# Kernel tuning notes

Hardware: AMD Instinct MI355X
Metric: run time of the kernel (lower is better)

Reference implementation:

```python
import jax, jax.numpy as jnp
import numpy as np

H, KVH, HD = 32, 8, 128          # query heads, kv heads, head_dim
HIDDEN = H * HD                   # 4096
TOTAL_KV = 3072                   # sum of (start_pos + seqlen) over the batch (static)
ROPE_THETA = 10000.0


def setup_inputs() -> dict:
    key = jax.random.key(0)
    ks = jax.random.split(key, 4)
    x = jax.random.normal(ks[0], (1024, HIDDEN), jnp.float32)
    wqkv = jax.random.normal(ks[1], (HIDDEN, HIDDEN + 2 * KVH * HD), jnp.float32) * 0.02
    wo = jax.random.normal(ks[2], (HIDDEN, HIDDEN), jnp.float32) * 0.02
    # paged cache: [num_layers=1, 2(k/v), cache_slots, kv_heads, head_dim], holds post-RoPE prefixes
    kv_cache = jax.random.normal(ks[3], (1, 2, 8192, KVH, HD), jnp.float32) * 0.02
    # 4 ragged requests: seqlens [512,256,128,128], cached prefixes [0,512,1024,512]
    seqstarts = jnp.array([0, 512, 768, 896, 1024], jnp.int32)
    start_pos = jnp.array([0, 512, 1024, 512], jnp.int32)
    kvstarts = jnp.array([0, 512, 1280, 2432, 3072], jnp.int32)  # cumsum of start_pos+seqlen
    cachestarts = jnp.array([0, 1024, 2560, 4096], jnp.int32)    # page base per request
    return dict(x=x, wqkv=wqkv, wo=wo, kv_cache=kv_cache, seqstarts=seqstarts,
                kvstarts=kvstarts, cachestarts=cachestarts, start_pos=start_pos)


def _rope(t, pos):
    # interleaved (GPT-J style) rotary over full head_dim; t: [T, nheads, HD], pos: [T]
    d2 = HD // 2
    inv_freq = 1.0 / (ROPE_THETA ** (jnp.arange(d2, dtype=jnp.float32) / d2))
    ang = pos.astype(jnp.float32)[:, None] * inv_freq      # [T, d2]
    cos = jnp.cos(ang)[:, None, :]
    sin = jnp.sin(ang)[:, None, :]
    x1, x2 = t[..., 0::2], t[..., 1::2]
    r1 = x1 * cos - x2 * sin
    r2 = x1 * sin + x2 * cos
    return jnp.stack([r1, r2], axis=-1).reshape(t.shape)


def _forward(x, wqkv, wo, kv_cache, seqstarts, kvstarts, cachestarts, start_pos):
    T = x.shape[0]
    # fused QKV projection
    xqkv = (x @ wqkv).reshape(T, H + 2 * KVH, HD)
    xq, xk, xv = jnp.split(xqkv, [H, H + KVH], axis=1)   # [T,32,HD],[T,8,HD],[T,8,HD]

    # per-token batch id and absolute position (ragged via seqstarts)
    tok = jnp.arange(T)
    bq = jnp.searchsorted(seqstarts, tok, side='right') - 1
    pos_q = tok - seqstarts[bq] + start_pos[bq]
    xq = _rope(xq, pos_q)
    xk = _rope(xk, pos_q)

    # assemble ragged KV stream: cached prefix (paged cache) + freshly projected tokens
    kvtok = jnp.arange(TOTAL_KV)
    bkv = jnp.searchsorted(kvstarts, kvtok, side='right') - 1
    pkv = kvtok - kvstarts[bkv]                              # absolute kv position
    is_new = pkv >= start_pos[bkv]
    new_idx = jnp.clip(seqstarts[bkv] + pkv - start_pos[bkv], 0, T - 1)
    cache_idx = cachestarts[bkv] + pkv                       # paged slot for prefix
    keys = jnp.where(is_new[:, None, None], xk[new_idx], kv_cache[0, 0][cache_idx])
    vals = jnp.where(is_new[:, None, None], xv[new_idx], kv_cache[0, 1][cache_idx])

    # GQA: repeat kv heads to match query heads
    rep = H // KVH
    keys = jnp.repeat(keys, rep, axis=1)                     # [TOTAL_KV, 32, HD]
    vals = jnp.repeat(vals, rep, axis=1)

    scale = 1.0 / jnp.sqrt(jnp.float32(HD))
    scores = jnp.einsum('qhd,khd->hqk', xq, keys) * scale    # [32, T, TOTAL_KV]
    # ragged causal mask: same request and kv position <= query position
    mask = (bq[:, None] == bkv[None, :]) & (pkv[None, :] <= pos_q[:, None])
    scores = jnp.where(mask[None], scores, jnp.float32(-1e30))
    probs = jax.nn.softmax(scores, axis=-1)
    attn = jnp.einsum('hqk,khd->qhd', probs, vals)           # [T, 32, HD]
    return attn.reshape(T, HIDDEN) @ wo


def reference(x, wqkv, wo, kv_cache, seqstarts, kvstarts, cachestarts, start_pos):
    return _forward(x, wqkv, wo, kv_cache, seqstarts, kvstarts, cachestarts, start_pos)
```

## Files before the change

kernel.cpp:

```cpp
#include <hip/hip_runtime.h>
#include <hip/hip_bf16.h>
#include <math.h>
#include <stdint.h>

typedef __bf16 bf16;
typedef __attribute__((ext_vector_type(4))) float floatx4;
typedef __attribute__((ext_vector_type(8))) bf16 bf16x8;
typedef __attribute__((ext_vector_type(4))) bf16 bf16x4;

#define LDS_ASYNC16(gptr, lptr)                                                \
  __builtin_amdgcn_global_load_lds(                                            \
      (const __attribute__((address_space(1))) void*)(gptr),                   \
      (__attribute__((address_space(3))) void*)(lptr), 16, 0, 0)

__global__ __launch_bounds__(256) void k_cvt(const float* __restrict__ in,
                                             bf16* __restrict__ out) {
  int i = (blockIdx.x * 256 + threadIdx.x) * 4;
  float4 v = *(const float4*)(in + i);
  bf16x4 o;
  o[0] = (bf16)v.x; o[1] = (bf16)v.y; o[2] = (bf16)v.z; o[3] = (bf16)v.w;
  *(bf16x4*)(out + i) = o;
}

__global__ __launch_bounds__(256) void k_merge(const float* __restrict__ a,
                                               const float* __restrict__ b,
                                               float* __restrict__ out) {
  int i = (blockIdx.x * 256 + threadIdx.x) * 4;
  float4 va = *(const float4*)(a + i);
  float4 vb = *(const float4*)(b + i);
  float4 o;
  o.x = va.x + vb.x; o.y = va.y + vb.y; o.z = va.z + vb.z; o.w = va.w + vb.w;
  *(float4*)(out + i) = o;
}

__global__ __launch_bounds__(256) void k_transpose_cvt(const float* __restrict__ in,
                                                       bf16* __restrict__ out,
                                                       int K, int N) {
  __shared__ float tile[64][65];
  int k0 = blockIdx.y * 64, n0 = blockIdx.x * 64;
  int tid = threadIdx.x;
  int cg = tid & 15, rr = tid >> 4;
#pragma unroll
  for (int p = 0; p < 4; ++p) {
    int r = rr + p * 16;
    float4 v = *(const float4*)(in + (size_t)(k0 + r) * N + n0 + cg * 4);
    tile[r][cg * 4 + 0] = v.x; tile[r][cg * 4 + 1] = v.y;
    tile[r][cg * 4 + 2] = v.z; tile[r][cg * 4 + 3] = v.w;
  }
  __syncthreads();
#pragma unroll
  for (int p = 0; p < 4; ++p) {
    int n = rr + p * 16;
    bf16x4 o;
    o[0] = (bf16)tile[cg * 4 + 0][n];
    o[1] = (bf16)tile[cg * 4 + 1][n];
    o[2] = (bf16)tile[cg * 4 + 2][n];
    o[3] = (bf16)tile[cg * 4 + 3][n];
    *(bf16x4*)(out + (size_t)(n0 + n) * K + k0 + cg * 4) = o;
  }
}

__global__ __launch_bounds__(256) void k_gemm_bt(const bf16* __restrict__ A,
                                                 const bf16* __restrict__ B,
                                                 float* __restrict__ C,
                                                 int M, int N, int K, int ksplit) {
  __shared__ bf16 As[128 * 32];
  __shared__ bf16 Bs[128 * 32];
  int tid = threadIdx.x;
  int w = tid >> 6, lane = tid & 63;
  int lq = lane >> 4, l16 = lane & 15;
  int bm = blockIdx.y * 128, bn = blockIdx.x * 128;
  int wm = (w >> 1) * 64, wn = (w & 1) * 64;
  int kc = K / ksplit;
  int koff = blockIdx.z * kc;
  C += (size_t)blockIdx.z * M * N;
  floatx4 acc[4][4] = {};
  const bf16* Ab = A + (size_t)bm * K;
  const bf16* Bb = B + (size_t)bn * K;
  int srow = (lane >> 2);
  int scol = (lane & 3) * 8;

  for (int k0 = koff; k0 < koff + kc; k0 += 32) {
#pragma unroll
    for (int c = 0; c < 2; ++c) {
      int r = w * 32 + c * 16 + srow;
      LDS_ASYNC16(Ab + (size_t)r * K + k0 + scol, &As[(w * 32 + c * 16) * 32]);
      LDS_ASYNC16(Bb + (size_t)r * K + k0 + scol, &Bs[(w * 32 + c * 16) * 32]);
    }
    __syncthreads();
    bf16x8 af[4], bfr[4];
#pragma unroll
    for (int i = 0; i < 4; ++i)
      af[i] = *(const bf16x8*)&As[(wm + i * 16 + l16) * 32 + lq * 8];
#pragma unroll
    for (int j = 0; j < 4; ++j)
      bfr[j] = *(const bf16x8*)&Bs[(wn + j * 16 + l16) * 32 + lq * 8];
#pragma unroll
    for (int i = 0; i < 4; ++i)
#pragma unroll
      for (int j = 0; j < 4; ++j)
        acc[i][j] = __builtin_amdgcn_mfma_f32_16x16x32_bf16(af[i], bfr[j],
                                                            acc[i][j], 0, 0, 0);
    __syncthreads();
  }
#pragma unroll
  for (int i = 0; i < 4; ++i)
#pragma unroll
    for (int j = 0; j < 4; ++j) {
      int m = bm + wm + i * 16 + lq * 4;
      int n = bn + wn + j * 16 + l16;
      float* cp = C + (size_t)m * N + n;
#pragma unroll
      for (int r = 0; r < 4; ++r) cp[(size_t)r * N] = acc[i][j][r];
    }
}

__global__ __launch_bounds__(256) void k_rope(const float* __restrict__ xp0,
                                              const float* __restrict__ xp1,
                                              bf16* __restrict__ qb,
                                              bf16* __restrict__ kb,
                                              const int* __restrict__ seqstarts,
                                              const int* __restrict__ start_pos) {
  int t = blockIdx.x;
  int s = 0;
  for (int i = 1; i < 4; ++i) if (seqstarts[i] <= t) s = i;
  float pos = (float)(t - seqstarts[s] + start_pos[s]);
  for (int wk = threadIdx.x; wk < 40 * 64; wk += 256) {
    int hh = wk >> 6, j = wk & 63;
    size_t idx = ((size_t)t * 48 + hh) * 128 + 2 * j;
    float x1 = xp0[idx] + xp1[idx];
    float x2 = xp0[idx + 1] + xp1[idx + 1];
    float invf = exp2f(-(float)j * 0.20762050593045935f);
    float ang = pos * invf;
    float sv, cv;
    sincosf(ang, &sv, &cv);
    float r1 = x1 * cv - x2 * sv;
    float r2 = x1 * sv + x2 * cv;
    unsigned int u1 = (unsigned int)__builtin_bit_cast(unsigned short, (bf16)r1);
    unsigned int u2 = (unsigned int)__builtin_bit_cast(unsigned short, (bf16)r2);
    unsigned int pk = u1 | (u2 << 16);
    unsigned int* dst = (hh < 32)
        ? (unsigned int*)(qb + ((size_t)t * 32 + hh) * 128)
        : (unsigned int*)(kb + ((size_t)t * 8 + (hh - 32)) * 128);
    dst[j] = pk;
  }
}

__global__ __launch_bounds__(256) void k_assemble_k(
    const bf16* __restrict__ xk, const float* __restrict__ ck,
    bf16* __restrict__ kall,
    const int* __restrict__ seqstarts, const int* __restrict__ kvstarts,
    const int* __restrict__ cachestarts, const int* __restrict__ start_pos) {
  int p = blockIdx.x;
  int b = 0;
  for (int i = 1; i < 4; ++i) if (kvstarts[i] <= p) b = i;
  int pkv = p - kvstarts[b];
  int tid = threadIdx.x;
  int hk = tid >> 5, d4 = (tid & 31) * 4;
  bf16* dst = kall + ((size_t)hk * 3072 + p) * 128 + d4;
  if (pkv >= start_pos[b]) {
    int tn = seqstarts[b] + pkv - start_pos[b];
    *(bf16x4*)dst = *(const bf16x4*)(xk + ((size_t)tn * 8 + hk) * 128 + d4);
  } else {
    int ci = cachestarts[b] + pkv;
    float4 v = *(const float4*)(ck + ((size_t)ci * 8 + hk) * 128 + d4);
    bf16x4 o;
    o[0] = (bf16)v.x; o[1] = (bf16)v.y; o[2] = (bf16)v.z; o[3] = (bf16)v.w;
    *(bf16x4*)dst = o;
  }
}

__global__ __launch_bounds__(256) void k_assemble_vT(
    const float* __restrict__ xp0, const float* __restrict__ xp1,
    const float* __restrict__ cv, bf16* __restrict__ vT,
    const int* __restrict__ seqstarts, const int* __restrict__ kvstarts,
    const int* __restrict__ cachestarts, const int* __restrict__ start_pos) {
  __shared__ float tile[64][130];
  int hk = blockIdx.y, p0 = blockIdx.x * 64;
  int tid = threadIdx.x;
  {
    int r = tid >> 2;
    int p = p0 + r;
    int b = 0;
    for (int i = 1; i < 4; ++i) if (kvstarts[i] <= p) b = i;
    int pkv = p - kvstarts[b];
    int f0 = (tid & 3) * 32;
    if (pkv >= start_pos[b]) {
      int tn = seqstarts[b] + pkv - start_pos[b];
      size_t base = (size_t)tn * 6144 + (40 + hk) * 128;
#pragma unroll
      for (int i = 0; i < 8; ++i) {
        float4 v0 = *(const float4*)(xp0 + base + f0 + i * 4);
        float4 v1 = *(const float4*)(xp1 + base + f0 + i * 4);
        tile[r][f0 + i * 4 + 0] = v0.x + v1.x;
        tile[r][f0 + i * 4 + 1] = v0.y + v1.y;
        tile[r][f0 + i * 4 + 2] = v0.z + v1.z;
        tile[r][f0 + i * 4 + 3] = v0.w + v1.w;
      }
    } else {
      int ci = cachestarts[b] + pkv;
      const float* src = cv + ((size_t)ci * 8 + hk) * 128;
#pragma unroll
      for (int i = 0; i < 8; ++i) {
        float4 v = *(const float4*)(src + f0 + i * 4);
        tile[r][f0 + i * 4 + 0] = v.x; tile[r][f0 + i * 4 + 1] = v.y;
        tile[r][f0 + i * 4 + 2] = v.z; tile[r][f0 + i * 4 + 3] = v.w;
      }
    }
  }
  __syncthreads();
  int d = tid >> 1, hf = tid & 1;
  bf16* dst = vT + ((size_t)hk * 128 + d) * 3072 + p0 + hf * 32;
#pragma unroll
  for (int q = 0; q < 4; ++q) {
    bf16x8 o;
#pragma unroll
    for (int e = 0; e < 8; ++e) o[e] = (bf16)tile[hf * 32 + q * 8 + e][d];
    *(bf16x8*)(dst + q * 8) = o;
  }
}

__global__ __launch_bounds__(256) void k_attn(
    const bf16* __restrict__ qb, const bf16* __restrict__ kall,
    const bf16* __restrict__ vT, bf16* __restrict__ aout,
    const int* __restrict__ seqstarts, const int* __restrict__ kvstarts,
    const int* __restrict__ start_pos) {
  __shared__ bf16 Qs[64 * 128];
  __shared__ bf16 Ks[64 * 128];
  __shared__ bf16 Vs[128 * 64];
  __shared__ bf16 Ps[64 * 64];
  int qbi = blockIdx.x, h = blockIdx.y, hk = h >> 2;
  int t0 = qbi * 64;
  int s = 0;
  for (int i = 1; i < 4; ++i) if (seqstarts[i] <= t0) s = i;
  int posbase = t0 - seqstarts[s] + start_pos[s];
  int kv0 = kvstarts[s];
  int nkv = posbase + 64;
  int tid = threadIdx.x, w = tid >> 6, lane = tid & 63;
  int lq = lane >> 4, l16 = lane & 15;

#pragma unroll
  for (int c = 0; c < 4; ++c) {
    int r = w * 16 + c * 4 + (lane >> 4);
    LDS_ASYNC16(qb + (((size_t)(t0 + r) * 32 + h) * 128 + (lane & 15) * 8),
                &Qs[(w * 16 + c * 4) * 128]);
  }
  float m_r[4], l_r[4];
  floatx4 oacc[8] = {};
#pragma unroll
  for (int rg = 0; rg < 4; ++rg) { m_r[rg] = -3.0e38f; l_r[rg] = 0.f; }
  const float scale = 0.08838834764831845f;

  for (int p0 = 0; p0 < nkv; p0 += 64) {
#pragma unroll
    for (int c = 0; c < 4; ++c) {
      int r = w * 16 + c * 4 + (lane >> 4);
      LDS_ASYNC16(kall + (((size_t)hk * 3072 + kv0 + p0 + r) * 128 + (lane & 15) * 8),
                  &Ks[(w * 16 + c * 4) * 128]);
    }
#pragma unroll
    for (int c = 0; c < 4; ++c) {
      int d = w * 32 + c * 8 + (lane >> 3);
      LDS_ASYNC16(vT + (((size_t)hk * 128 + d) * 3072 + kv0 + p0 + (lane & 7) * 8),
                  &Vs[(w * 32 + c * 8) * 64]);
    }
    __syncthreads();

    bf16x8 qa[4];
#pragma unroll
    for (int kk = 0; kk < 4; ++kk)
      qa[kk] = *(const bf16x8*)&Qs[(w * 16 + l16) * 128 + kk * 32 + lq * 8];
    floatx4 sacc[4] = {};
#pragma unroll
    for (int kk = 0; kk < 4; ++kk)
#pragma unroll
      for (int j = 0; j < 4; ++j) {
        bf16x8 kb = *(const bf16x8*)&Ks[(j * 16 + l16) * 128 + kk * 32 + lq * 8];
        sacc[j] = __builtin_amdgcn_mfma_f32_16x16x32_bf16(qa[kk], kb, sacc[j], 0, 0, 0);
      }

#pragma unroll
    for (int rg = 0; rg < 4; ++rg) {
      int qpos = posbase + w * 16 + lq * 4 + rg;
      float sv[4];
      float rmax = -3.0e38f;
#pragma unroll
      for (int j = 0; j < 4; ++j) {
        int pkv = p0 + j * 16 + l16;
        sv[j] = (pkv <= qpos) ? sacc[j][rg] * scale : -3.0e38f;
        rmax = fmaxf(rmax, sv[j]);
      }
#pragma unroll
      for (int off = 1; off < 16; off <<= 1)
        rmax = fmaxf(rmax, __shfl_xor(rmax, off, 64));
      float mnew = fmaxf(m_r[rg], rmax);
      float alpha = __expf(m_r[rg] - mnew);
      m_r[rg] = mnew;
      float psum = 0.f;
#pragma unroll
      for (int j = 0; j < 4; ++j) {
        float pv = __expf(sv[j] - mnew);
        psum += pv;
        Ps[(w * 16 + lq * 4 + rg) * 64 + j * 16 + l16] = (bf16)pv;
      }
#pragma unroll
      for (int off = 1; off < 16; off <<= 1) psum += __shfl_xor(psum, off, 64);
      l_r[rg] = l_r[rg] * alpha + psum;
#pragma unroll
      for (int nt = 0; nt < 8; ++nt) oacc[nt][rg] *= alpha;
    }

#pragma unroll
    for (int kk = 0; kk < 2; ++kk) {
      bf16x8 pa = *(const bf16x8*)&Ps[(w * 16 + l16) * 64 + kk * 32 + lq * 8];
#pragma unroll
      for (int nt = 0; nt < 8; ++nt) {
        bf16x8 vb = *(const bf16x8*)&Vs[(nt * 16 + l16) * 64 + kk * 32 + lq * 8];
        oacc[nt] = __builtin_amdgcn_mfma_f32_16x16x32_bf16(pa, vb, oacc[nt], 0, 0, 0);
      }
    }
    __syncthreads();
  }

#pragma unroll
  for (int rg = 0; rg < 4; ++rg) {
    float inv = 1.0f / l_r[rg];
    int t = t0 + w * 16 + lq * 4 + rg;
#pragma unroll
    for (int nt = 0; nt < 8; ++nt)
      aout[(size_t)t * 4096 + h * 128 + nt * 16 + l16] =
          (bf16)(oacc[nt][rg] * inv);
  }
}

extern "C" void kernel_launch(void* const* d_in, const int* in_sizes, int n_in,
                              void* d_out, int out_size, void* d_ws, size_t ws_size,
                              hipStream_t stream) {
  const float* x = (const float*)d_in[0];
  const float* wqkv = (const float*)d_in[1];
  const float* wo = (const float*)d_in[2];
  const float* kv = (const float*)d_in[3];
  const int* seqstarts = (const int*)d_in[4];
  const int* kvstarts = (const int*)d_in[5];
  const int* cachestarts = (const int*)d_in[6];
  const int* start_pos = (const int*)d_in[7];
  float* out = (float*)d_out;

  char* base = (char*)d_ws;
  size_t off = 0;
  auto carve = [&](size_t bytes) {
    void* r = base + off;
    off += (bytes + 255) & ~(size_t)255;
    return r;
  };
  bf16* x_bf    = (bf16*)carve(1024ull * 4096 * 2);
  bf16* wqkvT   = (bf16*)carve(6144ull * 4096 * 2);
  bf16* woT     = (bf16*)carve(4096ull * 4096 * 2);
  float* xqkv   = (float*)carve(2ull * 1024 * 6144 * 4);
  bf16* q_bf    = (bf16*)carve(1024ull * 32 * 128 * 2);
  bf16* xk_bf   = (bf16*)carve(1024ull * 8 * 128 * 2);
  bf16* k_all   = (bf16*)carve(8ull * 3072 * 128 * 2);
  bf16* vT_all  = (bf16*)carve(8ull * 128 * 3072 * 2);
  bf16* attn_bf = (bf16*)carve(1024ull * 4096 * 2);
  float* outp = (float*)wqkvT;

  float* xqkv1 = xqkv + 1024ull * 6144;
  const float* cache_v = kv + 8192ull * 8 * 128;

  k_cvt<<<4096, 256, 0, stream>>>(x, x_bf);
  k_transpose_cvt<<<dim3(96, 64), 256, 0, stream>>>(wqkv, wqkvT, 4096, 6144);
  k_transpose_cvt<<<dim3(64, 64), 256, 0, stream>>>(wo, woT, 4096, 4096);
  k_gemm_bt<<<dim3(48, 8, 2), 256, 0, stream>>>(x_bf, wqkvT, xqkv, 1024, 6144,
                                                4096, 2);
  k_rope<<<1024, 256, 0, stream>>>(xqkv, xqkv1, q_bf, xk_bf, seqstarts, start_pos);
  k_assemble_k<<<3072, 256, 0, stream>>>(xk_bf, kv, k_all, seqstarts, kvstarts,
                                         cachestarts, start_pos);
  k_assemble_vT<<<dim3(48, 8), 256, 0, stream>>>(xqkv, xqkv1, cache_v, vT_all,
                                                 seqstarts, kvstarts, cachestarts,
                                                 start_pos);
  k_attn<<<dim3(16, 32), 256, 0, stream>>>(q_bf, k_all, vT_all, attn_bf,
                                           seqstarts, kvstarts, start_pos);
  k_gemm_bt<<<dim3(32, 8, 2), 256, 0, stream>>>(attn_bf, woT, outp, 1024, 4096,
                                                4096, 2);
  k_merge<<<4096, 256, 0, stream>>>(outp, outp + 1024ull * 4096, out);
}
```

Before: 507.1 us.

## XOR-swizzle LDS layouts in GEMM and attention, keep Q in registers

```diff
diff --git a/kernel.cpp b/kernel.cpp
--- a/kernel.cpp
+++ b/kernel.cpp
@@ -78,7 +78,8 @@
   const bf16* Ab = A + (size_t)bm * K;
   const bf16* Bb = B + (size_t)bn * K;
   int srow = (lane >> 2);
-  int scol = (lane & 3) * 8;
+  int scol = (((lane & 3) ^ ((srow >> 1) & 3))) * 8;
+  int sa = (l16 >> 1) & 3;
 
   for (int k0 = koff; k0 < koff + kc; k0 += 32) {
 #pragma unroll
@@ -91,10 +92,10 @@
     bf16x8 af[4], bfr[4];
 #pragma unroll
     for (int i = 0; i < 4; ++i)
-      af[i] = *(const bf16x8*)&As[(wm + i * 16 + l16) * 32 + lq * 8];
+      af[i] = *(const bf16x8*)&As[(wm + i * 16 + l16) * 32 + (lq ^ sa) * 8];
 #pragma unroll
     for (int j = 0; j < 4; ++j)
-      bfr[j] = *(const bf16x8*)&Bs[(wn + j * 16 + l16) * 32 + lq * 8];
+      bfr[j] = *(const bf16x8*)&Bs[(wn + j * 16 + l16) * 32 + (lq ^ sa) * 8];
 #pragma unroll
     for (int i = 0; i < 4; ++i)
 #pragma unroll
@@ -128,8 +129,10 @@
   for (int wk = threadIdx.x; wk < 40 * 64; wk += 256) {
     int hh = wk >> 6, j = wk & 63;
     size_t idx = ((size_t)t * 48 + hh) * 128 + 2 * j;
-    float x1 = xp0[idx] + xp1[idx];
-    float x2 = xp0[idx + 1] + xp1[idx + 1];
+    float2 a0 = *(const float2*)(xp0 + idx);
+    float2 a1 = *(const float2*)(xp1 + idx);
+    float x1 = a0.x + a1.x;
+    float x2 = a0.y + a1.y;
     float invf = exp2f(-(float)j * 0.20762050593045935f);
     float ang = pos * invf;
     float sv, cv;
@@ -220,12 +223,11 @@
   }
 }
 
-__global__ __launch_bounds__(256) void k_attn(
+__global__ __launch_bounds__(256, 4) void k_attn(
     const bf16* __restrict__ qb, const bf16* __restrict__ kall,
     const bf16* __restrict__ vT, bf16* __restrict__ aout,
     const int* __restrict__ seqstarts, const int* __restrict__ kvstarts,
     const int* __restrict__ start_pos) {
-  __shared__ bf16 Qs[64 * 128];
   __shared__ bf16 Ks[64 * 128];
   __shared__ bf16 Vs[128 * 64];
   __shared__ bf16 Ps[64 * 64];
@@ -239,12 +241,18 @@
   int tid = threadIdx.x, w = tid >> 6, lane = tid & 63;
   int lq = lane >> 4, l16 = lane & 15;
 
-#pragma unroll
-  for (int c = 0; c < 4; ++c) {
-    int r = w * 16 + c * 4 + (lane >> 4);
-    LDS_ASYNC16(qb + (((size_t)(t0 + r) * 32 + h) * 128 + (lane & 15) * 8),
-                &Qs[(w * 16 + c * 4) * 128]);
-  }
+  bf16x8 qa[4];
+#pragma unroll
+  for (int kk = 0; kk < 4; ++kk)
+    qa[kk] = *(const bf16x8*)(qb + (((size_t)(t0 + w * 16 + l16) * 32 + h) * 128 +
+                                    kk * 32 + lq * 8));
+
+  int krow = lane >> 4;
+  int kchunk = ((lane & 15) ^ krow) ;
+  int vrow = lane >> 3;
+  int vchunk = ((lane & 7) ^ (vrow & 7));
+  int sw8 = l16 & 7;
+
   float m_r[4], l_r[4];
   floatx4 oacc[8] = {};
 #pragma unroll
@@ -254,28 +262,28 @@
   for (int p0 = 0; p0 < nkv; p0 += 64) {
 #pragma unroll
     for (int c = 0; c < 4; ++c) {
-      int r = w * 16 + c * 4 + (lane >> 4);
-      LDS_ASYNC16(kall + (((size_t)hk * 3072 + kv0 + p0 + r) * 128 + (lane & 15) * 8),
-                  &Ks[(w * 16 + c * 4) * 128]);
+      int base_r = w * 16 + c * 4;
+      int r = base_r + krow;
+      int gch = (lane & 15) ^ ((c * 4 + krow) & 15);
+      LDS_ASYNC16(kall + (((size_t)hk * 3072 + kv0 + p0 + r) * 128 + gch * 8),
+                  &Ks[base_r * 128]);
     }
 #pragma unroll
     for (int c = 0; c < 4; ++c) {
-      int d = w * 32 + c * 8 + (lane >> 3);
-      LDS_ASYNC16(vT + (((size_t)hk * 128 + d) * 3072 + kv0 + p0 + (lane & 7) * 8),
-                  &Vs[(w * 32 + c * 8) * 64]);
+      int base_d = w * 32 + c * 8;
+      int d = base_d + vrow;
+      LDS_ASYNC16(vT + (((size_t)hk * 128 + d) * 3072 + kv0 + p0 + vchunk * 8),
+                  &Vs[base_d * 64]);
     }
     __syncthreads();
 
-    bf16x8 qa[4];
+    floatx4 sacc[4] = {};
 #pragma unroll
     for (int kk = 0; kk < 4; ++kk)
-      qa[kk] = *(const bf16x8*)&Qs[(w * 16 + l16) * 128 + kk * 32 + lq * 8];
-    floatx4 sacc[4] = {};
-#pragma unroll
-    for (int kk = 0; kk < 4; ++kk)
 #pragma unroll
       for (int j = 0; j < 4; ++j) {
-        bf16x8 kb = *(const bf16x8*)&Ks[(j * 16 + l16) * 128 + kk * 32 + lq * 8];
+        bf16x8 kb = *(const bf16x8*)&Ks[(j * 16 + l16) * 128 +
+                                        ((kk * 4 + lq) ^ l16) * 8];
         sacc[j] = __builtin_amdgcn_mfma_f32_16x16x32_bf16(qa[kk], kb, sacc[j], 0, 0, 0);
       }
 
@@ -296,12 +304,15 @@
       float mnew = fmaxf(m_r[rg], rmax);
       float alpha = __expf(m_r[rg] - mnew);
       m_r[rg] = mnew;
+      int prow = w * 16 + lq * 4 + rg;
+      int pswz = (lq * 4 + rg) & 7;
       float psum = 0.f;
 #pragma unroll
       for (int j = 0; j < 4; ++j) {
         float pv = __expf(sv[j] - mnew);
         psum += pv;
-        Ps[(w * 16 + lq * 4 + rg) * 64 + j * 16 + l16] = (bf16)pv;
+        int chunk = (j * 2 + (l16 >> 3)) ^ pswz;
+        Ps[prow * 64 + chunk * 8 + (l16 & 7)] = (bf16)pv;
       }
 #pragma unroll
       for (int off = 1; off < 16; off <<= 1) psum += __shfl_xor(psum, off, 64);
@@ -312,10 +323,12 @@
 
 #pragma unroll
     for (int kk = 0; kk < 2; ++kk) {
-      bf16x8 pa = *(const bf16x8*)&Ps[(w * 16 + l16) * 64 + kk * 32 + lq * 8];
+      bf16x8 pa = *(const bf16x8*)&Ps[(w * 16 + l16) * 64 +
+                                      ((kk * 4 + lq) ^ sw8) * 8];
 #pragma unroll
       for (int nt = 0; nt < 8; ++nt) {
-        bf16x8 vb = *(const bf16x8*)&Vs[(nt * 16 + l16) * 64 + kk * 32 + lq * 8];
+        bf16x8 vb = *(const bf16x8*)&Vs[(nt * 16 + l16) * 64 +
+                                        ((kk * 4 + lq) ^ sw8) * 8];
         oacc[nt] = __builtin_amdgcn_mfma_f32_16x16x32_bf16(pa, vb, oacc[nt], 0, 0, 0);
       }
     }
```

New measurement: 517.2 us. About the same (+2.0%).
